# Kernel tuning notes

Measured on AMD Instinct MI355X. Metric: run time of the kernel, lower is better.

## Reference

```python
import jax, jax.numpy as jnp
import numpy as np

N_NODES = 100000
N_EDGES = 1600000
C_IN = 32
C_OUT = 32


def setup_inputs() -> dict:
    key = jax.random.key(0)
    ks = jax.random.split(key, 12)
    x = jax.random.normal(ks[0], (N_NODES, C_IN), dtype=jnp.float32)
    edge_index = jax.random.randint(ks[1], (2, N_EDGES), 0, N_NODES, dtype=jnp.int64)
    def glorot(k, fan_in, fan_out):
        s = jnp.sqrt(6.0 / (fan_in + fan_out))
        return jax.random.uniform(k, (fan_in, fan_out), jnp.float32, -s, s)
    return {
        "x": x,
        "edge_index": edge_index,
        "W1": glorot(ks[2], C_IN, C_OUT),  "b1": jnp.zeros((C_OUT,), jnp.float32),
        "W2": glorot(ks[3], C_OUT, C_OUT), "b2": jnp.zeros((C_OUT,), jnp.float32),
        "Wmu": glorot(ks[4], C_OUT, C_OUT), "bmu": jnp.zeros((C_OUT,), jnp.float32),
        "Wlv": glorot(ks[5], C_OUT, C_OUT), "blv": jnp.zeros((C_OUT,), jnp.float32),
    }


def _gcn_norm(edge_index, n_nodes):
    # PyG GCNConv default: add self-loops, symmetric normalization.
    loops = jnp.arange(n_nodes, dtype=edge_index.dtype)
    src = jnp.concatenate([edge_index[0], loops])
    dst = jnp.concatenate([edge_index[1], loops])
    deg = jax.ops.segment_sum(jnp.ones_like(dst, dtype=jnp.float32), dst,
                              num_segments=n_nodes)
    dis = jnp.where(deg > 0, jax.lax.rsqrt(deg), 0.0)  # deg^-1/2
    norm = dis[src] * dis[dst]  # [E + N]
    return src, dst, norm


def _gcn_layer(x, src, dst, norm, W, b, n_nodes):
    h = x @ W                                   # [N, Cout]
    msg = h[src] * norm[:, None]                # gather + scale, [E+N, Cout]
    out = jax.ops.segment_sum(msg, dst, num_segments=n_nodes)  # scatter-add
    return out + b


def reference(x, edge_index, W1, b1, W2, b2, Wmu, bmu, Wlv, blv):
    n = x.shape[0]
    src, dst, norm = _gcn_norm(edge_index, n)
    h = jax.nn.relu(_gcn_layer(x, src, dst, norm, W1, b1, n))
    h = jax.nn.relu(_gcn_layer(h, src, dst, norm, W2, b2, n))
    mu = _gcn_layer(h, src, dst, norm, Wmu, bmu, n)
    logvar = _gcn_layer(h, src, dst, norm, Wlv, blv, n)
    return (mu, logvar)
```

## Files before the change

### kernel.cpp

```cpp
#include <hip/hip_runtime.h>
#include <hip/hip_fp16.h>


#define BK_BITS 9
#define BK      (1 << BK_BITS)
#define BMASK   (BK - 1)
#define EPT     16
#define CHUNK   (256 * EPT)
#define CAP     16384

typedef int   vint4   __attribute__((ext_vector_type(4)));
typedef uint  vuint4  __attribute__((ext_vector_type(4)));
typedef float vfloat4 __attribute__((ext_vector_type(4)));

#define NTL(p) __builtin_nontemporal_load(p)

__global__ void k_bucket(const int* __restrict__ src, const int* __restrict__ dst,
                         int* __restrict__ bcur, int* __restrict__ ebuf, int E) {
    __shared__ int lcnt[256];
    __shared__ int lbase[256];
    int t = threadIdx.x;
    lcnt[t] = 0;
    __syncthreads();
    int e0 = blockIdx.x * CHUNK;
    int pk[EPT];
#pragma unroll
    for (int i = 0; i < EPT; ++i) {
        int e = e0 + i * 256 + t;
        pk[i] = -1;
        if (e < E) {
            int d = NTL(dst + e);
            int b = d >> BK_BITS;
            int off = atomicAdd(&lcnt[b], 1);
            pk[i] = (b << 21) | (off << BK_BITS) | (d & BMASK);
        }
    }
    __syncthreads();
    lbase[t] = t * CAP + atomicAdd(&bcur[t], lcnt[t]);
    __syncthreads();
#pragma unroll
    for (int i = 0; i < EPT; ++i) {
        int e = e0 + i * 256 + t;
        if (e < E) {
            int b   = pk[i] >> 21;
            int off = (pk[i] >> BK_BITS) & 4095;
            int dl  = pk[i] & BMASK;
            int pos = lbase[b] + off;
            if (pos < (b + 1) * CAP)
                ebuf[pos] = (NTL(src + e) << BK_BITS) | dl;
        }
    }
}

__global__ void k_finalize(const int* __restrict__ bcur, int* __restrict__ starts,
                           float* __restrict__ dis, const int* __restrict__ ebuf,
                           int* __restrict__ es, const float* __restrict__ x,
                           __half* __restrict__ g0, int n, int E) {
    __shared__ int   hist[BK];
    __shared__ int   sc[BK];
    __shared__ int   sb[256];
    __shared__ float disL[BK];
    int b = blockIdx.x, t = threadIdx.x;
    if (t < 256) sb[t] = min(bcur[t], CAP);
    hist[t] = 0;
    __syncthreads();
    for (int o = 1; o < 256; o <<= 1) {
        int xv = 0;
        if (t < 256 && t >= o) xv = sb[t - o];
        __syncthreads();
        if (t < 256) sb[t] += xv;
        __syncthreads();
    }
    int cnt = min(bcur[b], CAP);
    int beg = sb[b] - cnt;
    const int* eb = ebuf + (size_t)b * CAP;
    for (int j = t; j < cnt; j += BK)
        atomicAdd(&hist[eb[j] & BMASK], 1);
    __syncthreads();
    int cv = hist[t];
    sc[t] = cv;
    __syncthreads();
    for (int o = 1; o < BK; o <<= 1) {
        int xv = (t >= o) ? sc[t - o] : 0;
        __syncthreads();
        sc[t] += xv;
        __syncthreads();
    }
    int excl = sc[t] - cv;
    int gnode = (b << BK_BITS) + t;
    float dv = rsqrtf((float)cv + 1.0f);
    disL[t] = dv;
    if (gnode < n) {
        starts[gnode] = beg + excl;
        dis[gnode] = dv;
    }
    if (b == 0 && t == 0) starts[n] = E;
    hist[t] = excl;
    __syncthreads();
    for (int j = t; j < cnt; j += BK) {
        int v = eb[j];
        int off = atomicAdd(&hist[v & BMASK], 1);
        es[beg + off] = v >> BK_BITS;
    }
    int node0 = b << BK_BITS;
    const float4* x4 = (const float4*)x;
    uint2* g2 = (uint2*)g0;
    for (int idx = t; idx < BK * 8; idx += BK) {
        int r = idx >> 3, lane = idx & 7;
        int nd = node0 + r;
        if (nd < n) {
            float d = disL[r];
            float4 v = x4[(size_t)nd * 8 + lane];
            __half2 lo = __floats2half2_rn(d * v.x, d * v.y);
            __half2 hi = __floats2half2_rn(d * v.z, d * v.w);
            uint2 u;
            u.x = *(unsigned int*)&lo;
            u.y = *(unsigned int*)&hi;
            g2[(size_t)nd * 8 + lane] = u;
        }
    }
}

__device__ inline void acc8(uint4 u, float* s) {
    __half2 h0 = *(__half2*)&u.x, h1 = *(__half2*)&u.y;
    __half2 h2 = *(__half2*)&u.z, h3 = *(__half2*)&u.w;
    float2 f0 = __half22float2(h0), f1 = __half22float2(h1);
    float2 f2 = __half22float2(h2), f3 = __half22float2(h3);
    s[0] += f0.x; s[1] += f0.y; s[2] += f1.x; s[3] += f1.y;
    s[4] += f2.x; s[5] += f2.y; s[6] += f3.x; s[7] += f3.y;
}

__device__ inline void gather32(const int* __restrict__ starts,
                                const int* __restrict__ es,
                                const uint4* __restrict__ g4,
                                int node, int lane, float* s) {
    acc8(g4[(size_t)node * 4 + lane], s);
    int j = starts[node], end = starts[node + 1];
    while (j < end && (j & 3)) {
        acc8(g4[(size_t)es[j] * 4 + lane], s);
        ++j;
    }
    for (; j + 8 <= end; j += 8) {
        int4 e0 = *(const int4*)(es + j);
        int4 e1 = *(const int4*)(es + j + 4);
        uint4 u0 = g4[(size_t)e0.x * 4 + lane];
        uint4 u1 = g4[(size_t)e0.y * 4 + lane];
        uint4 u2 = g4[(size_t)e0.z * 4 + lane];
        uint4 u3 = g4[(size_t)e0.w * 4 + lane];
        uint4 u4 = g4[(size_t)e1.x * 4 + lane];
        uint4 u5 = g4[(size_t)e1.y * 4 + lane];
        uint4 u6 = g4[(size_t)e1.z * 4 + lane];
        uint4 u7 = g4[(size_t)e1.w * 4 + lane];
        acc8(u0, s); acc8(u1, s); acc8(u2, s); acc8(u3, s);
        acc8(u4, s); acc8(u5, s); acc8(u6, s); acc8(u7, s);
    }
    if (j + 4 <= end) {
        int4 e0 = *(const int4*)(es + j);
        uint4 u0 = g4[(size_t)e0.x * 4 + lane];
        uint4 u1 = g4[(size_t)e0.y * 4 + lane];
        uint4 u2 = g4[(size_t)e0.z * 4 + lane];
        uint4 u3 = g4[(size_t)e0.w * 4 + lane];
        acc8(u0, s); acc8(u1, s); acc8(u2, s); acc8(u3, s);
        j += 4;
    }
    for (; j < end; ++j) acc8(g4[(size_t)es[j] * 4 + lane], s);
}

__global__ __launch_bounds__(256)
void k_fused16(const int* __restrict__ starts, const int* __restrict__ es,
               const float* __restrict__ dis, const __half* __restrict__ g,
               const float* __restrict__ W, const float* __restrict__ bias,
               __half* __restrict__ gout, int n) {
    __shared__ float Ws[32][33];
    __shared__ float Xs[64][33];
    int t = threadIdx.x;
    for (int i = t; i < 1024; i += 256) Ws[i >> 5][i & 31] = W[i];
    int r = t >> 2, lane = t & 3;
    int node = blockIdx.x * 64 + r;
    bool alive = node < n;
    float dd = 0.f;
    if (alive) {
        float s[8] = {0, 0, 0, 0, 0, 0, 0, 0};
        gather32(starts, es, (const uint4*)g, node, lane, s);
        dd = dis[node];
#pragma unroll
        for (int i = 0; i < 8; ++i) Xs[r][lane * 8 + i] = dd * s[i];
    }
    __syncthreads();
    if (alive) {
        int c0 = lane * 8;
        float acc[8];
#pragma unroll
        for (int i = 0; i < 8; ++i) acc[i] = bias[c0 + i];
#pragma unroll 8
        for (int k = 0; k < 32; ++k) {
            float xv = Xs[r][k];
#pragma unroll
            for (int i = 0; i < 8; ++i) acc[i] += xv * Ws[k][c0 + i];
        }
        __half2 h0 = __floats2half2_rn(dd * fmaxf(acc[0], 0.f), dd * fmaxf(acc[1], 0.f));
        __half2 h1 = __floats2half2_rn(dd * fmaxf(acc[2], 0.f), dd * fmaxf(acc[3], 0.f));
        __half2 h2 = __floats2half2_rn(dd * fmaxf(acc[4], 0.f), dd * fmaxf(acc[5], 0.f));
        __half2 h3 = __floats2half2_rn(dd * fmaxf(acc[6], 0.f), dd * fmaxf(acc[7], 0.f));
        uint4 u;
        u.x = *(unsigned int*)&h0; u.y = *(unsigned int*)&h1;
        u.z = *(unsigned int*)&h2; u.w = *(unsigned int*)&h3;
        ((uint4*)gout)[(size_t)node * 4 + lane] = u;
    }
}

__global__ __launch_bounds__(256)
void k_fused_final(const int* __restrict__ starts, const int* __restrict__ es,
                   const float* __restrict__ dis, const __half* __restrict__ g,
                   const float* __restrict__ Wmu, const float* __restrict__ Wlv,
                   const float* __restrict__ bmu, const float* __restrict__ blv,
                   float* __restrict__ out, int n) {
    __shared__ float Ws[32][66];
    __shared__ float Xs[64][33];
    int t = threadIdx.x;
    for (int i = t; i < 1024; i += 256) {
        Ws[i >> 5][i & 31]        = Wmu[i];
        Ws[i >> 5][32 + (i & 31)] = Wlv[i];
    }
    int r = t >> 2, lane = t & 3;
    int node = blockIdx.x * 64 + r;
    bool alive = node < n;
    if (alive) {
        float s[8] = {0, 0, 0, 0, 0, 0, 0, 0};
        gather32(starts, es, (const uint4*)g, node, lane, s);
        float dd = dis[node];
#pragma unroll
        for (int i = 0; i < 8; ++i) Xs[r][lane * 8 + i] = dd * s[i];
    }
    __syncthreads();
    if (alive) {
        int c0 = lane * 8;
        float am[8], al[8];
#pragma unroll
        for (int i = 0; i < 8; ++i) { am[i] = bmu[c0 + i]; al[i] = blv[c0 + i]; }
#pragma unroll 4
        for (int k = 0; k < 32; ++k) {
            float xv = Xs[r][k];
#pragma unroll
            for (int i = 0; i < 8; ++i) {
                am[i] += xv * Ws[k][c0 + i];
                al[i] += xv * Ws[k][32 + c0 + i];
            }
        }
        float4* om = (float4*)out + (size_t)node * 8 + lane * 2;
        om[0] = make_float4(am[0], am[1], am[2], am[3]);
        om[1] = make_float4(am[4], am[5], am[6], am[7]);
        float4* ol = (float4*)(out + (size_t)n * 32) + (size_t)node * 8 + lane * 2;
        ol[0] = make_float4(al[0], al[1], al[2], al[3]);
        ol[1] = make_float4(al[4], al[5], al[6], al[7]);
    }
}


extern "C" void kernel_launch(void* const* d_in, const int* in_sizes, int n_in,
                              void* d_out, int out_size, void* d_ws, size_t ws_size,
                              hipStream_t stream) {
    const float* x   = (const float*)d_in[0];
    const int*   ei  = (const int*)d_in[1];
    const float* W1  = (const float*)d_in[2];
    const float* b1  = (const float*)d_in[3];
    const float* W2  = (const float*)d_in[4];
    const float* b2  = (const float*)d_in[5];
    const float* Wmu = (const float*)d_in[6];
    const float* bmu = (const float*)d_in[7];
    const float* Wlv = (const float*)d_in[8];
    const float* blv = (const float*)d_in[9];
    float* out = (float*)d_out;

    int n = in_sizes[0] / 32;
    int E = in_sizes[1] / 2;
    const int* src = ei;
    const int* dst = ei + E;
    int nbuck = (n + BK - 1) >> BK_BITS;

    int*    bcur   = (int*)d_ws;
    int     npad   = (n + 4) & ~3;
    int*    starts = bcur + 256;
    float*  dis    = (float*)(starts + npad);
    int*    es     = (int*)(dis + n);
    __half* gA     = (__half*)(es + E);
    __half* gB     = gA + (size_t)n * 32;
    int*    ebuf   = (int*)(gB + (size_t)n * 32);

    int nblk  = (E + CHUNK - 1) / CHUNK;
    int agrid = (n + 63) / 64;

    hipMemsetAsync(bcur, 0, 256 * sizeof(int), stream);
    k_bucket<<<nblk, 256, 0, stream>>>(src, dst, bcur, ebuf, E);
    k_finalize<<<nbuck, BK, 0, stream>>>(bcur, starts, dis, ebuf, es, x, gA, n, E);

    k_fused16<<<agrid, 256, 0, stream>>>(starts, es, dis, gA, W1, b1, gB, n);
    k_fused16<<<agrid, 256, 0, stream>>>(starts, es, dis, gB, W2, b2, gA, n);
    k_fused_final<<<agrid, 256, 0, stream>>>(starts, es, dis, gA, Wmu, Wlv, bmu, blv, out, n);
}
```

Baseline: 249.2 us.

## Fuse three GCN layer kernels into one persistent cooperative kernel with grid sync

Replaces the three separate layer launches with a single cooperative persistent kernel. Tiles are handed out dynamically through atomic counters, and grid.sync separates the layers. This is meant to remove launch gaps and tail effects between layers and to balance uneven node degrees. In exchange it adds grid-wide barriers and per-tile atomics, and it caps the grid at an occupancy-based size that assumes 256 CUs.

After: 517.4 us. 2.08x slower.

```diff
diff --git a/kernel.cpp b/kernel.cpp
--- a/kernel.cpp
+++ b/kernel.cpp
@@ -1,5 +1,8 @@
 #include <hip/hip_runtime.h>
 #include <hip/hip_fp16.h>
+#include <hip/hip_cooperative_groups.h>
+
+namespace cg = cooperative_groups;
 
 
 #define BK_BITS 9
@@ -166,94 +169,130 @@
     for (; j < end; ++j) acc8(g4[(size_t)es[j] * 4 + lane], s);
 }
 
-__global__ __launch_bounds__(256)
-void k_fused16(const int* __restrict__ starts, const int* __restrict__ es,
-               const float* __restrict__ dis, const __half* __restrict__ g,
-               const float* __restrict__ W, const float* __restrict__ bias,
-               __half* __restrict__ gout, int n) {
-    __shared__ float Ws[32][33];
-    __shared__ float Xs[64][33];
+__device__ __forceinline__ void hidden_phase(
+        const int* __restrict__ starts, const int* __restrict__ es,
+        const float* __restrict__ dis, const __half* __restrict__ g,
+        const float* __restrict__ W, const float* __restrict__ bias,
+        __half* __restrict__ gout, int n, int ntiles, int* __restrict__ tctr,
+        float (*Ws)[66], float (*Xs)[33], int* tileShared) {
     int t = threadIdx.x;
     for (int i = t; i < 1024; i += 256) Ws[i >> 5][i & 31] = W[i];
-    int r = t >> 2, lane = t & 3;
-    int node = blockIdx.x * 64 + r;
-    bool alive = node < n;
-    float dd = 0.f;
-    if (alive) {
+    int r = t >> 2, lane = t & 3, c0 = lane * 8;
+    float bc[8];
+#pragma unroll
+    for (int i = 0; i < 8; ++i) bc[i] = bias[c0 + i];
+    for (;;) {
+        if (t == 0) *tileShared = atomicAdd(tctr, 1);
+        __syncthreads();
+        int tile = *tileShared;
+        if (tile >= ntiles) break;
+        int node = tile * 64 + r;
+        bool alive = node < n;
+        float dd = 0.f;
         float s[8] = {0, 0, 0, 0, 0, 0, 0, 0};
-        gather32(starts, es, (const uint4*)g, node, lane, s);
-        dd = dis[node];
-#pragma unroll
-        for (int i = 0; i < 8; ++i) Xs[r][lane * 8 + i] = dd * s[i];
-    }
-    __syncthreads();
-    if (alive) {
-        int c0 = lane * 8;
-        float acc[8];
-#pragma unroll
-        for (int i = 0; i < 8; ++i) acc[i] = bias[c0 + i];
+        if (alive) {
+            gather32(starts, es, (const uint4*)g, node, lane, s);
+            dd = dis[node];
+#pragma unroll
+            for (int i = 0; i < 8; ++i) Xs[r][c0 + i] = dd * s[i];
+        }
+        __syncthreads();
+        if (alive) {
+            float acc[8];
+#pragma unroll
+            for (int i = 0; i < 8; ++i) acc[i] = bc[i];
 #pragma unroll 8
-        for (int k = 0; k < 32; ++k) {
-            float xv = Xs[r][k];
-#pragma unroll
-            for (int i = 0; i < 8; ++i) acc[i] += xv * Ws[k][c0 + i];
-        }
-        __half2 h0 = __floats2half2_rn(dd * fmaxf(acc[0], 0.f), dd * fmaxf(acc[1], 0.f));
-        __half2 h1 = __floats2half2_rn(dd * fmaxf(acc[2], 0.f), dd * fmaxf(acc[3], 0.f));
-        __half2 h2 = __floats2half2_rn(dd * fmaxf(acc[4], 0.f), dd * fmaxf(acc[5], 0.f));
-        __half2 h3 = __floats2half2_rn(dd * fmaxf(acc[6], 0.f), dd * fmaxf(acc[7], 0.f));
-        uint4 u;
-        u.x = *(unsigned int*)&h0; u.y = *(unsigned int*)&h1;
-        u.z = *(unsigned int*)&h2; u.w = *(unsigned int*)&h3;
-        ((uint4*)gout)[(size_t)node * 4 + lane] = u;
-    }
-}
-
-__global__ __launch_bounds__(256)
-void k_fused_final(const int* __restrict__ starts, const int* __restrict__ es,
-                   const float* __restrict__ dis, const __half* __restrict__ g,
-                   const float* __restrict__ Wmu, const float* __restrict__ Wlv,
-                   const float* __restrict__ bmu, const float* __restrict__ blv,
-                   float* __restrict__ out, int n) {
-    __shared__ float Ws[32][66];
-    __shared__ float Xs[64][33];
+            for (int k = 0; k < 32; ++k) {
+                float xv = Xs[r][k];
+#pragma unroll
+                for (int i = 0; i < 8; ++i) acc[i] += xv * Ws[k][c0 + i];
+            }
+            __half2 h0 = __floats2half2_rn(dd * fmaxf(acc[0], 0.f), dd * fmaxf(acc[1], 0.f));
+            __half2 h1 = __floats2half2_rn(dd * fmaxf(acc[2], 0.f), dd * fmaxf(acc[3], 0.f));
+            __half2 h2 = __floats2half2_rn(dd * fmaxf(acc[4], 0.f), dd * fmaxf(acc[5], 0.f));
+            __half2 h3 = __floats2half2_rn(dd * fmaxf(acc[6], 0.f), dd * fmaxf(acc[7], 0.f));
+            uint4 u;
+            u.x = *(unsigned int*)&h0; u.y = *(unsigned int*)&h1;
+            u.z = *(unsigned int*)&h2; u.w = *(unsigned int*)&h3;
+            ((uint4*)gout)[(size_t)node * 4 + lane] = u;
+        }
+    }
+}
+
+__device__ __forceinline__ void final_phase(
+        const int* __restrict__ starts, const int* __restrict__ es,
+        const float* __restrict__ dis, const __half* __restrict__ g,
+        const float* __restrict__ Wmu, const float* __restrict__ Wlv,
+        const float* __restrict__ bmu, const float* __restrict__ blv,
+        float* __restrict__ out, int n, int ntiles, int* __restrict__ tctr,
+        float (*Ws)[66], float (*Xs)[33], int* tileShared) {
     int t = threadIdx.x;
     for (int i = t; i < 1024; i += 256) {
         Ws[i >> 5][i & 31]        = Wmu[i];
         Ws[i >> 5][32 + (i & 31)] = Wlv[i];
     }
-    int r = t >> 2, lane = t & 3;
-    int node = blockIdx.x * 64 + r;
-    bool alive = node < n;
-    if (alive) {
+    int r = t >> 2, lane = t & 3, c0 = lane * 8;
+    float bm[8], bl[8];
+#pragma unroll
+    for (int i = 0; i < 8; ++i) { bm[i] = bmu[c0 + i]; bl[i] = blv[c0 + i]; }
+    for (;;) {
+        if (t == 0) *tileShared = atomicAdd(tctr, 1);
+        __syncthreads();
+        int tile = *tileShared;
+        if (tile >= ntiles) break;
+        int node = tile * 64 + r;
+        bool alive = node < n;
+        float dd = 0.f;
         float s[8] = {0, 0, 0, 0, 0, 0, 0, 0};
-        gather32(starts, es, (const uint4*)g, node, lane, s);
-        float dd = dis[node];
-#pragma unroll
-        for (int i = 0; i < 8; ++i) Xs[r][lane * 8 + i] = dd * s[i];
-    }
-    __syncthreads();
-    if (alive) {
-        int c0 = lane * 8;
-        float am[8], al[8];
-#pragma unroll
-        for (int i = 0; i < 8; ++i) { am[i] = bmu[c0 + i]; al[i] = blv[c0 + i]; }
+        if (alive) {
+            gather32(starts, es, (const uint4*)g, node, lane, s);
+            dd = dis[node];
+#pragma unroll
+            for (int i = 0; i < 8; ++i) Xs[r][c0 + i] = dd * s[i];
+        }
+        __syncthreads();
+        if (alive) {
+            float am[8], al[8];
+#pragma unroll
+            for (int i = 0; i < 8; ++i) { am[i] = bm[i]; al[i] = bl[i]; }
 #pragma unroll 4
-        for (int k = 0; k < 32; ++k) {
-            float xv = Xs[r][k];
-#pragma unroll
-            for (int i = 0; i < 8; ++i) {
-                am[i] += xv * Ws[k][c0 + i];
-                al[i] += xv * Ws[k][32 + c0 + i];
+            for (int k = 0; k < 32; ++k) {
+                float xv = Xs[r][k];
+#pragma unroll
+                for (int i = 0; i < 8; ++i) {
+                    am[i] += xv * Ws[k][c0 + i];
+                    al[i] += xv * Ws[k][32 + c0 + i];
+                }
             }
-        }
-        float4* om = (float4*)out + (size_t)node * 8 + lane * 2;
-        om[0] = make_float4(am[0], am[1], am[2], am[3]);
-        om[1] = make_float4(am[4], am[5], am[6], am[7]);
-        float4* ol = (float4*)(out + (size_t)n * 32) + (size_t)node * 8 + lane * 2;
-        ol[0] = make_float4(al[0], al[1], al[2], al[3]);
-        ol[1] = make_float4(al[4], al[5], al[6], al[7]);
-    }
+            float4* om = (float4*)out + (size_t)node * 8 + lane * 2;
+            om[0] = make_float4(am[0], am[1], am[2], am[3]);
+            om[1] = make_float4(am[4], am[5], am[6], am[7]);
+            float4* ol = (float4*)(out + (size_t)n * 32) + (size_t)node * 8 + lane * 2;
+            ol[0] = make_float4(al[0], al[1], al[2], al[3]);
+            ol[1] = make_float4(al[4], al[5], al[6], al[7]);
+        }
+    }
+}
+
+__global__ __launch_bounds__(256, 4)
+void k_layers(const int* starts, const int* es, const float* dis,
+              __half* gA, __half* gB,
+              const float* W1, const float* b1,
+              const float* W2, const float* b2,
+              const float* Wmu, const float* Wlv,
+              const float* bmu, const float* blv,
+              float* out, int* tctr, int n, int ntiles) {
+    __shared__ float Ws[32][66];
+    __shared__ float Xs[64][33];
+    __shared__ int   tileShared;
+    cg::grid_group grid = cg::this_grid();
+    hidden_phase(starts, es, dis, gA, W1, b1, gB, n, ntiles, tctr + 0, Ws, Xs, &tileShared);
+    __threadfence();
+    grid.sync();
+    hidden_phase(starts, es, dis, gB, W2, b2, gA, n, ntiles, tctr + 1, Ws, Xs, &tileShared);
+    __threadfence();
+    grid.sync();
+    final_phase(starts, es, dis, gA, Wmu, Wlv, bmu, blv, out, n, ntiles, tctr + 2, Ws, Xs, &tileShared);
 }
 
 
@@ -279,22 +318,33 @@
     int nbuck = (n + BK - 1) >> BK_BITS;
 
     int*    bcur   = (int*)d_ws;
+    int*    tctr   = bcur + 256;
     int     npad   = (n + 4) & ~3;
-    int*    starts = bcur + 256;
+    int*    starts = bcur + 272;
     float*  dis    = (float*)(starts + npad);
     int*    es     = (int*)(dis + n);
     __half* gA     = (__half*)(es + E);
     __half* gB     = gA + (size_t)n * 32;
     int*    ebuf   = (int*)(gB + (size_t)n * 32);
 
-    int nblk  = (E + CHUNK - 1) / CHUNK;
-    int agrid = (n + 63) / 64;
-
-    hipMemsetAsync(bcur, 0, 256 * sizeof(int), stream);
+    int nblk   = (E + CHUNK - 1) / CHUNK;
+    int ntiles = (n + 63) / 64;
+
+    hipMemsetAsync(bcur, 0, 272 * sizeof(int), stream);
     k_bucket<<<nblk, 256, 0, stream>>>(src, dst, bcur, ebuf, E);
     k_finalize<<<nbuck, BK, 0, stream>>>(bcur, starts, dis, ebuf, es, x, gA, n, E);
 
-    k_fused16<<<agrid, 256, 0, stream>>>(starts, es, dis, gA, W1, b1, gB, n);
-    k_fused16<<<agrid, 256, 0, stream>>>(starts, es, dis, gB, W2, b2, gA, n);
-    k_fused_final<<<agrid, 256, 0, stream>>>(starts, es, dis, gA, Wmu, Wlv, bmu, blv, out, n);
-}
+    static int coopBlocks = 0;
+    if (coopBlocks == 0) {
+        int mb = 0;
+        if (hipOccupancyMaxActiveBlocksPerMultiprocessor(&mb, k_layers, 256, 0) != hipSuccess || mb < 1)
+            mb = 4;
+        coopBlocks = mb * 256;
+    }
+    int cgrid = coopBlocks < ntiles ? coopBlocks : ntiles;
+    void* kargs[] = {(void*)&starts, (void*)&es, (void*)&dis, (void*)&gA, (void*)&gB,
+                     (void*)&W1, (void*)&b1, (void*)&W2, (void*)&b2,
+                     (void*)&Wmu, (void*)&Wlv, (void*)&bmu, (void*)&blv,
+                     (void*)&out, (void*)&tctr, (void*)&n, (void*)&ntiles};
+    hipLaunchCooperativeKernel(k_layers, dim3(cgrid), dim3(256), kargs, 0, stream);
+}
```

## Sort nodes by degree within each bucket to balance gather work

Applied to the files above, without the earlier changes.

In the finalize kernel, each bucket of 512 nodes is counting-sorted by in-degree (clamped to 63) in descending order, and the resulting node permutation is written to a new perm array. The three aggregation kernels look up their node through perm, so the nodes in a wavefront have similar degrees and lanes spend less time idle on divergent loop lengths. In exchange there is an extra indirection per thread, slightly less coalesced output and gather-source writes, extra shared-memory atomics in finalize, and a small extra workspace. Padded slots past n carry gnode >= n, so they fail the alive check and are skipped.

Measured after the change: 281.8 us. 1.13x slower.

```diff
diff --git a/kernel.cpp b/kernel.cpp
--- a/kernel.cpp
+++ b/kernel.cpp
@@ -55,14 +55,19 @@
 __global__ void k_finalize(const int* __restrict__ bcur, int* __restrict__ starts,
                            float* __restrict__ dis, const int* __restrict__ ebuf,
                            int* __restrict__ es, const float* __restrict__ x,
-                           __half* __restrict__ g0, int n, int E) {
+                           __half* __restrict__ g0, int* __restrict__ perm,
+                           int n, int E) {
     __shared__ int   hist[BK];
     __shared__ int   sc[BK];
     __shared__ int   sb[256];
     __shared__ float disL[BK];
+    __shared__ int   dh[64];
+    __shared__ int   db[64];
+    __shared__ int   dc[64];
     int b = blockIdx.x, t = threadIdx.x;
     if (t < 256) sb[t] = min(bcur[t], CAP);
     hist[t] = 0;
+    if (t < 64) { dh[t] = 0; dc[t] = 0; }
     __syncthreads();
     for (int o = 1; o < 256; o <<= 1) {
         int xv = 0;
@@ -95,6 +100,17 @@
         dis[gnode] = dv;
     }
     if (b == 0 && t == 0) starts[n] = E;
+    int dcl = min(cv, 63);
+    atomicAdd(&dh[dcl], 1);
+    __syncthreads();
+    if (t < 64) {
+        int v = 0;
+        for (int d = t + 1; d < 64; ++d) v += dh[d];
+        db[t] = v;
+    }
+    __syncthreads();
+    int rank = db[dcl] + atomicAdd(&dc[dcl], 1);
+    perm[(b << BK_BITS) + rank] = gnode;
     hist[t] = excl;
     __syncthreads();
     for (int j = t; j < cnt; j += BK) {
@@ -170,13 +186,13 @@
 void k_fused16(const int* __restrict__ starts, const int* __restrict__ es,
                const float* __restrict__ dis, const __half* __restrict__ g,
                const float* __restrict__ W, const float* __restrict__ bias,
-               __half* __restrict__ gout, int n) {
+               __half* __restrict__ gout, const int* __restrict__ perm, int n) {
     __shared__ float Ws[32][33];
     __shared__ float Xs[64][33];
     int t = threadIdx.x;
     for (int i = t; i < 1024; i += 256) Ws[i >> 5][i & 31] = W[i];
     int r = t >> 2, lane = t & 3;
-    int node = blockIdx.x * 64 + r;
+    int node = perm[blockIdx.x * 64 + r];
     bool alive = node < n;
     float dd = 0.f;
     if (alive) {
@@ -214,7 +230,7 @@
                    const float* __restrict__ dis, const __half* __restrict__ g,
                    const float* __restrict__ Wmu, const float* __restrict__ Wlv,
                    const float* __restrict__ bmu, const float* __restrict__ blv,
-                   float* __restrict__ out, int n) {
+                   float* __restrict__ out, const int* __restrict__ perm, int n) {
     __shared__ float Ws[32][66];
     __shared__ float Xs[64][33];
     int t = threadIdx.x;
@@ -223,7 +239,7 @@
         Ws[i >> 5][32 + (i & 31)] = Wlv[i];
     }
     int r = t >> 2, lane = t & 3;
-    int node = blockIdx.x * 64 + r;
+    int node = perm[blockIdx.x * 64 + r];
     bool alive = node < n;
     if (alive) {
         float s[8] = {0, 0, 0, 0, 0, 0, 0, 0};
@@ -285,16 +301,17 @@
     int*    es     = (int*)(dis + n);
     __half* gA     = (__half*)(es + E);
     __half* gB     = gA + (size_t)n * 32;
-    int*    ebuf   = (int*)(gB + (size_t)n * 32);
+    int*    perm   = (int*)(gB + (size_t)n * 32);
+    int*    ebuf   = perm + (size_t)nbuck * BK;
 
     int nblk  = (E + CHUNK - 1) / CHUNK;
-    int agrid = (n + 63) / 64;
+    int agrid = nbuck * (BK / 64);
 
     hipMemsetAsync(bcur, 0, 256 * sizeof(int), stream);
     k_bucket<<<nblk, 256, 0, stream>>>(src, dst, bcur, ebuf, E);
-    k_finalize<<<nbuck, BK, 0, stream>>>(bcur, starts, dis, ebuf, es, x, gA, n, E);
-
-    k_fused16<<<agrid, 256, 0, stream>>>(starts, es, dis, gA, W1, b1, gB, n);
-    k_fused16<<<agrid, 256, 0, stream>>>(starts, es, dis, gB, W2, b2, gA, n);
-    k_fused_final<<<agrid, 256, 0, stream>>>(starts, es, dis, gA, Wmu, Wlv, bmu, blv, out, n);
-}
+    k_finalize<<<nbuck, BK, 0, stream>>>(bcur, starts, dis, ebuf, es, x, gA, perm, n, E);
+
+    k_fused16<<<agrid, 256, 0, stream>>>(starts, es, dis, gA, W1, b1, gB, perm, n);
+    k_fused16<<<agrid, 256, 0, stream>>>(starts, es, dis, gB, W2, b2, gA, perm, n);
+    k_fused_final<<<agrid, 256, 0, stream>>>(starts, es, dis, gA, Wmu, Wlv, bmu, blv, out, perm, n);
+}
```

## Split CSR finalize per bucket across eight blocks and widen bucketing blocks

Applied to the files above, without the earlier changes.

The finalize stage now launches eight 256-thread blocks per 512-node bucket instead of one 512-thread block. Each block recomputes the bucket histogram and prefix sum redundantly, then scatters only the edges and node features for its 64-node slice. The bucketing kernel moves to 512 threads with 8 edges per thread. This aims to spread the finalize work over more CUs, at the cost of each block re-reading the whole bucket's edge buffer eight times.

New measurement: 255.9 us. 2.7% more time.

```diff
diff --git a/kernel.cpp b/kernel.cpp
--- a/kernel.cpp
+++ b/kernel.cpp
@@ -5,8 +5,9 @@
 #define BK_BITS 9
 #define BK      (1 << BK_BITS)
 #define BMASK   (BK - 1)
-#define EPT     16
-#define CHUNK   (256 * EPT)
+#define BTHR    512
+#define EPT     8
+#define CHUNK   (BTHR * EPT)
 #define CAP     16384
 
 typedef int   vint4   __attribute__((ext_vector_type(4)));
@@ -15,18 +16,19 @@
 
 #define NTL(p) __builtin_nontemporal_load(p)
 
-__global__ void k_bucket(const int* __restrict__ src, const int* __restrict__ dst,
-                         int* __restrict__ bcur, int* __restrict__ ebuf, int E) {
+__global__ __launch_bounds__(BTHR)
+void k_bucket(const int* __restrict__ src, const int* __restrict__ dst,
+              int* __restrict__ bcur, int* __restrict__ ebuf, int E) {
     __shared__ int lcnt[256];
     __shared__ int lbase[256];
     int t = threadIdx.x;
-    lcnt[t] = 0;
+    if (t < 256) lcnt[t] = 0;
     __syncthreads();
     int e0 = blockIdx.x * CHUNK;
     int pk[EPT];
 #pragma unroll
     for (int i = 0; i < EPT; ++i) {
-        int e = e0 + i * 256 + t;
+        int e = e0 + i * BTHR + t;
         pk[i] = -1;
         if (e < E) {
             int d = NTL(dst + e);
@@ -36,11 +38,11 @@
         }
     }
     __syncthreads();
-    lbase[t] = t * CAP + atomicAdd(&bcur[t], lcnt[t]);
+    if (t < 256) lbase[t] = t * CAP + atomicAdd(&bcur[t], lcnt[t]);
     __syncthreads();
 #pragma unroll
     for (int i = 0; i < EPT; ++i) {
-        int e = e0 + i * 256 + t;
+        int e = e0 + i * BTHR + t;
         if (e < E) {
             int b   = pk[i] >> 21;
             int off = (pk[i] >> BK_BITS) & 4095;
@@ -52,71 +54,86 @@
     }
 }
 
-__global__ void k_finalize(const int* __restrict__ bcur, int* __restrict__ starts,
-                           float* __restrict__ dis, const int* __restrict__ ebuf,
-                           int* __restrict__ es, const float* __restrict__ x,
-                           __half* __restrict__ g0, int n, int E) {
+__global__ __launch_bounds__(256)
+void k_finalize2(const int* __restrict__ bcur, int* __restrict__ starts,
+                 float* __restrict__ dis, const int* __restrict__ ebuf,
+                 int* __restrict__ es, const float* __restrict__ x,
+                 __half* __restrict__ g0, int n, int E) {
+    __shared__ int   sb[256];
     __shared__ int   hist[BK];
-    __shared__ int   sc[BK];
-    __shared__ int   sb[256];
-    __shared__ float disL[BK];
-    int b = blockIdx.x, t = threadIdx.x;
-    if (t < 256) sb[t] = min(bcur[t], CAP);
-    hist[t] = 0;
+    __shared__ int   hsc[BK];
+    __shared__ int   curs[64];
+    __shared__ float disw[64];
+    int b = blockIdx.x >> 3;
+    int w = blockIdx.x & 7;
+    int t = threadIdx.x;
+    sb[t] = min(bcur[t], CAP);
     __syncthreads();
     for (int o = 1; o < 256; o <<= 1) {
-        int xv = 0;
-        if (t < 256 && t >= o) xv = sb[t - o];
+        int v = (t >= o) ? sb[t - o] : 0;
         __syncthreads();
-        if (t < 256) sb[t] += xv;
+        sb[t] += v;
         __syncthreads();
     }
     int cnt = min(bcur[b], CAP);
     int beg = sb[b] - cnt;
+    hist[t] = 0; hist[t + 256] = 0;
+    __syncthreads();
     const int* eb = ebuf + (size_t)b * CAP;
-    for (int j = t; j < cnt; j += BK)
+    for (int j = t; j < cnt; j += 256)
         atomicAdd(&hist[eb[j] & BMASK], 1);
     __syncthreads();
-    int cv = hist[t];
-    sc[t] = cv;
-    __syncthreads();
-    for (int o = 1; o < BK; o <<= 1) {
-        int xv = (t >= o) ? sc[t - o] : 0;
+    int a0 = hist[2 * t], a1 = hist[2 * t + 1];
+    int ps = a0 + a1;
+    sb[t] = ps;
+    __syncthreads();
+    for (int o = 1; o < 256; o <<= 1) {
+        int v = (t >= o) ? sb[t - o] : 0;
         __syncthreads();
-        sc[t] += xv;
+        sb[t] += v;
         __syncthreads();
     }
-    int excl = sc[t] - cv;
-    int gnode = (b << BK_BITS) + t;
-    float dv = rsqrtf((float)cv + 1.0f);
-    disL[t] = dv;
-    if (gnode < n) {
-        starts[gnode] = beg + excl;
-        dis[gnode] = dv;
-    }
-    if (b == 0 && t == 0) starts[n] = E;
-    hist[t] = excl;
-    __syncthreads();
-    for (int j = t; j < cnt; j += BK) {
+    int ebase = sb[t] - ps;
+    hsc[2 * t]     = ebase;
+    hsc[2 * t + 1] = ebase + a0;
+    __syncthreads();
+    if (t < 64) {
+        int r = w * 64 + t;
+        int gnode = (b << BK_BITS) + r;
+        int cv = hist[r];
+        float dv = rsqrtf((float)cv + 1.0f);
+        disw[t] = dv;
+        if (gnode < n) {
+            starts[gnode] = beg + hsc[r];
+            dis[gnode] = dv;
+        }
+        curs[t] = hsc[r];
+    }
+    if (blockIdx.x == 0 && t == 0) starts[n] = E;
+    __syncthreads();
+    for (int j = t; j < cnt; j += 256) {
         int v = eb[j];
-        int off = atomicAdd(&hist[v & BMASK], 1);
-        es[beg + off] = v >> BK_BITS;
-    }
-    int node0 = b << BK_BITS;
+        int dl = v & BMASK;
+        if ((dl >> 6) == w) {
+            int off = atomicAdd(&curs[dl & 63], 1);
+            es[beg + off] = v >> BK_BITS;
+        }
+    }
+    int node0 = (b << BK_BITS) + w * 64;
     const float4* x4 = (const float4*)x;
     uint2* g2 = (uint2*)g0;
-    for (int idx = t; idx < BK * 8; idx += BK) {
-        int r = idx >> 3, lane = idx & 7;
+    for (int idx = t; idx < 64 * 8; idx += 256) {
+        int r = idx >> 3, ln = idx & 7;
         int nd = node0 + r;
         if (nd < n) {
-            float d = disL[r];
-            float4 v = x4[(size_t)nd * 8 + lane];
+            float d = disw[r];
+            float4 v = x4[(size_t)nd * 8 + ln];
             __half2 lo = __floats2half2_rn(d * v.x, d * v.y);
             __half2 hi = __floats2half2_rn(d * v.z, d * v.w);
             uint2 u;
             u.x = *(unsigned int*)&lo;
             u.y = *(unsigned int*)&hi;
-            g2[(size_t)nd * 8 + lane] = u;
+            g2[(size_t)nd * 8 + ln] = u;
         }
     }
 }
@@ -291,8 +308,8 @@
     int agrid = (n + 63) / 64;
 
     hipMemsetAsync(bcur, 0, 256 * sizeof(int), stream);
-    k_bucket<<<nblk, 256, 0, stream>>>(src, dst, bcur, ebuf, E);
-    k_finalize<<<nbuck, BK, 0, stream>>>(bcur, starts, dis, ebuf, es, x, gA, n, E);
+    k_bucket<<<nblk, BTHR, 0, stream>>>(src, dst, bcur, ebuf, E);
+    k_finalize2<<<nbuck * 8, 256, 0, stream>>>(bcur, starts, dis, ebuf, es, x, gA, n, E);
 
     k_fused16<<<agrid, 256, 0, stream>>>(starts, es, dis, gA, W1, b1, gB, n);
     k_fused16<<<agrid, 256, 0, stream>>>(starts, es, dis, gB, W2, b2, gA, n);
```
